# Kernel optimization log

Measured on AMD Instinct MI355X. Metric: run time of the kernel, lower is better.

## Reference

```python
import jax, jax.numpy as jnp
import numpy as np

N = 100000
E = 1600000
D = 128
EPS = 1e-5


def setup_inputs() -> dict:
    key = jax.random.key(0)
    ks = jax.random.split(key, 6)
    X = jax.random.normal(ks[0], (N, D), dtype=jnp.float32)
    edge_weight = jax.random.uniform(ks[1], (E,), dtype=jnp.float32)
    W = jax.random.normal(ks[2], (2 * D, D), dtype=jnp.float32) * (1.0 / np.sqrt(2 * D))
    b = jax.random.normal(ks[3], (D,), dtype=jnp.float32) * 0.01
    gamma = jnp.ones((D,), dtype=jnp.float32)
    beta = jnp.zeros((D,), dtype=jnp.float32)
    edge_src = jax.random.randint(ks[4], (E,), 0, N, dtype=jnp.int32)
    edge_dst = jax.random.randint(ks[5], (E,), 0, N, dtype=jnp.int32)
    return {"X": X, "edge_weight": edge_weight, "W": W, "b": b,
            "gamma": gamma, "beta": beta,
            "edge_src": edge_src, "edge_dst": edge_dst}


def reference(X, edge_weight, W, b, gamma, beta, edge_src, edge_dst):
    # Pre-LayerNorm over feature dim
    mu = jnp.mean(X, axis=-1, keepdims=True)
    var = jnp.mean(jnp.square(X - mu), axis=-1, keepdims=True)
    H = (X - mu) * jax.lax.rsqrt(var + EPS) * gamma + beta
    # dropout is identity in eval mode
    # sparse neighbor aggregation: neigh[i] = sum_{e: dst[e]=i} w[e] * H[src[e]]
    msgs = edge_weight[:, None] * H[edge_src]          # [E, D]
    neigh = jax.ops.segment_sum(msgs, edge_dst, num_segments=X.shape[0])  # [N, D]
    cat = jnp.concatenate([H, neigh], axis=1)          # [N, 2D]
    out = cat @ W + b                                  # [N, D]
    out = jax.nn.relu(out)
    return out + X                                     # residual (in_dim == out_dim)
```

## Files before the change

kernel.cpp:

```cpp
#include <hip/hip_runtime.h>
#include <hip/hip_bf16.h>

#define N_NODES 100000
#define D 128
#define E_EDGES 1600000

#define BSHIFT 6
#define BROWS 64
#define NBUCK 1563
#define CAP 1536
#define NBLK_S 256
#define EPB (E_EDGES / NBLK_S)
#define LN_BLOCKS (N_NODES / 4)

typedef __attribute__((ext_vector_type(8))) short bf16x8;
typedef __attribute__((ext_vector_type(4))) float f32x4;

__device__ __forceinline__ float bf2f(unsigned short u) {
    unsigned int x = ((unsigned int)u) << 16;
    return __builtin_bit_cast(float, x);
}
__device__ __forceinline__ unsigned short f2bf(float f) {
    unsigned int x = __builtin_bit_cast(unsigned int, f);
    unsigned int lsb = (x >> 16) & 1u;
    x += 0x7fffu + lsb;
    return (unsigned short)(x >> 16);
}

__global__ __launch_bounds__(256) void fused_ln_scatter(
    const float* __restrict__ X,
    const float* __restrict__ gamma,
    const float* __restrict__ beta,
    unsigned short* __restrict__ H,
    const int* __restrict__ esrc, const int* __restrict__ edst,
    const float* __restrict__ ew,
    unsigned int* __restrict__ gcur,
    uint2* __restrict__ bins)
{
    __shared__ unsigned int h[NBUCK];

    if (blockIdx.x < NBLK_S) {
        const int t = threadIdx.x;
        for (int i = t; i < NBUCK; i += 256) h[i] = 0;
        __syncthreads();

        const int base = blockIdx.x * EPB;
        for (int k = t; k < EPB; k += 256)
            atomicAdd(&h[edst[base + k] >> BSHIFT], 1u);
        __syncthreads();

        for (int i = t; i < NBUCK; i += 256) {
            unsigned int c = h[i];
            h[i] = c ? atomicAdd(&gcur[i], c) : 0u;
        }
        __syncthreads();

        for (int k = t; k < EPB; k += 256) {
            int e = base + k;
            int d = edst[e];
            int bkt = d >> BSHIFT;
            unsigned int p = atomicAdd(&h[bkt], 1u);
            if (p < CAP)
                bins[(size_t)bkt * CAP + p] =
                    make_uint2((unsigned int)esrc[e] |
                               ((unsigned int)(d & (BROWS - 1)) << 17),
                               __builtin_bit_cast(unsigned int, ew[e]));
        }
    } else {
        int wid  = ((blockIdx.x - NBLK_S) * 256 + threadIdx.x) >> 6;
        int lane = threadIdx.x & 63;
        if (wid >= N_NODES) return;

        const float2 x2 = *reinterpret_cast<const float2*>(X + (size_t)wid * D + 2 * lane);
        float x0 = x2.x, x1 = x2.y;
        float s  = x0 + x1;
        float sq = x0 * x0 + x1 * x1;
        #pragma unroll
        for (int m = 1; m < 64; m <<= 1) {
            s  += __shfl_xor(s,  m);
            sq += __shfl_xor(sq, m);
        }
        float mu   = s * (1.0f / 128.0f);
        float var  = sq * (1.0f / 128.0f) - mu * mu;
        float rstd = rsqrtf(var + 1e-5f);

        const float2 g2 = *reinterpret_cast<const float2*>(gamma + 2 * lane);
        const float2 b2 = *reinterpret_cast<const float2*>(beta  + 2 * lane);

        ushort2 h2;
        h2.x = f2bf((x0 - mu) * rstd * g2.x + b2.x);
        h2.y = f2bf((x1 - mu) * rstd * g2.y + b2.y);
        *reinterpret_cast<ushort2*>(H + (size_t)wid * D + 2 * lane) = h2;
    }
}

__global__ __launch_bounds__(256) void bucket_sort(
    uint2* __restrict__ bins,
    const unsigned int* __restrict__ gcur,
    uint2* __restrict__ offs2)
{
    __shared__ uint2 ent[CAP];
    __shared__ unsigned int cnt[BROWS];
    __shared__ unsigned int cur[BROWS];

    const int b = blockIdx.x;
    const int t = threadIdx.x;
    const unsigned int e0 = (unsigned int)b * CAP;
    const int nE = (int)min(gcur[b], (unsigned int)CAP);

    if (t < BROWS) cnt[t] = 0;
    __syncthreads();

    for (int k = t; k < nE; k += 256) {
        uint2 r = bins[e0 + k];
        ent[k] = r;
        atomicAdd(&cnt[r.x >> 17], 1u);
    }
    __syncthreads();

    if (t < BROWS) {
        unsigned int v = cnt[t], inc = v;
        #pragma unroll
        for (int off = 1; off < BROWS; off <<= 1) {
            unsigned int u = __shfl_up(inc, off);
            if (t >= off) inc += u;
        }
        unsigned int start = e0 + inc - v;
        cur[t] = start;
        int node = b * BROWS + t;
        if (node < N_NODES) offs2[node] = make_uint2(start, start + v);
    }
    __syncthreads();

    for (int k = t; k < nE; k += 256) {
        uint2 r = ent[k];
        unsigned int p = atomicAdd(&cur[r.x >> 17], 1u);
        bins[p] = make_uint2(r.x & 0x1FFFFu, r.y);
    }
}

__global__ __launch_bounds__(256) void aggregate_kernel(
    const unsigned short* __restrict__ H,
    const uint2* __restrict__ bins,
    const uint2* __restrict__ offs2,
    unsigned short* __restrict__ nb)
{
    int wid  = (blockIdx.x * blockDim.x + threadIdx.x) >> 6;
    int lane = threadIdx.x & 63;
    if (wid >= N_NODES) return;

    const uint2 o = offs2[wid];
    unsigned int e = o.x, e1 = o.y;
    float a0 = 0.f, a1 = 0.f;

    while (e + 8 <= e1) {
        uint2 r[8];
        #pragma unroll
        for (int j = 0; j < 8; ++j) r[j] = bins[e + j];
        ushort2 hh[8];
        #pragma unroll
        for (int j = 0; j < 8; ++j)
            hh[j] = *reinterpret_cast<const ushort2*>(H + (size_t)r[j].x * D + 2 * lane);
        #pragma unroll
        for (int j = 0; j < 8; ++j) {
            float w = __builtin_bit_cast(float, r[j].y);
            a0 += w * bf2f(hh[j].x);
            a1 += w * bf2f(hh[j].y);
        }
        e += 8;
    }
    if (e + 4 <= e1) {
        uint2 r[4];
        #pragma unroll
        for (int j = 0; j < 4; ++j) r[j] = bins[e + j];
        #pragma unroll
        for (int j = 0; j < 4; ++j) {
            float w = __builtin_bit_cast(float, r[j].y);
            ushort2 hh = *reinterpret_cast<const ushort2*>(H + (size_t)r[j].x * D + 2 * lane);
            a0 += w * bf2f(hh.x);
            a1 += w * bf2f(hh.y);
        }
        e += 4;
    }
    for (; e < e1; ++e) {
        uint2 r0 = bins[e];
        float w0 = __builtin_bit_cast(float, r0.y);
        ushort2 h0 = *reinterpret_cast<const ushort2*>(H + (size_t)r0.x * D + 2 * lane);
        a0 += w0 * bf2f(h0.x);
        a1 += w0 * bf2f(h0.y);
    }
    ushort2 ov;
    ov.x = f2bf(a0);
    ov.y = f2bf(a1);
    *reinterpret_cast<ushort2*>(nb + (size_t)wid * D + 2 * lane) = ov;
}

#define ROWS_PER_BLOCK 128
#define STRIPS 8

__global__ __launch_bounds__(256) void gemm_kernel(
    const unsigned short* __restrict__ H,
    const unsigned short* __restrict__ nb,
    const float* __restrict__ W,
    const float* __restrict__ bias,
    const float* __restrict__ X,
    float* __restrict__ out)
{
    __shared__ unsigned short lds[16][256];

    const int tid  = threadIdx.x;
    const int w    = tid >> 6;
    const int lane = tid & 63;
    const int l15  = lane & 15;
    const int l4   = lane >> 4;

    bf16x8 bfrag[2][8];
    #pragma unroll
    for (int t = 0; t < 2; ++t) {
        int col = 32 * w + 16 * t + l15;
        #pragma unroll
        for (int s = 0; s < 8; ++s) {
            bf16x8 v;
            #pragma unroll
            for (int j = 0; j < 8; ++j)
                v[j] = (short)f2bf(W[(32 * s + 8 * l4 + j) * D + col]);
            bfrag[t][s] = v;
        }
    }
    const float bias0 = bias[32 * w + l15];
    const float bias1 = bias[32 * w + 16 + l15];

    const int row0_blk = blockIdx.x * ROWS_PER_BLOCK;

    for (int strip = 0; strip < STRIPS; ++strip) {
        const int r0 = row0_blk + strip * 16;
        __syncthreads();

        {
            const int row  = tid >> 4;
            const int c8   = tid & 15;
            const int grow = r0 + row;
            char* ldsrow = (char*)&lds[row][0];
            const int key = (row & 7) << 4;

            uint4 hv = make_uint4(0u, 0u, 0u, 0u);
            uint4 nv = make_uint4(0u, 0u, 0u, 0u);
            if (grow < N_NODES) {
                hv = *reinterpret_cast<const uint4*>(H  + (size_t)grow * D + 8 * c8);
                nv = *reinterpret_cast<const uint4*>(nb + (size_t)grow * D + 8 * c8);
            }
            *reinterpret_cast<uint4*>(ldsrow + ((16 * c8) ^ key)) = hv;
            *reinterpret_cast<uint4*>(ldsrow + ((256 + 16 * c8) ^ key)) = nv;
        }
        __syncthreads();

        f32x4 acc0 = {0.f, 0.f, 0.f, 0.f};
        f32x4 acc1 = {0.f, 0.f, 0.f, 0.f};
        const char* ldsa = (const char*)&lds[l15][0];
        const int   akey = (l15 & 7) << 4;
        #pragma unroll
        for (int s = 0; s < 8; ++s) {
            bf16x8 afrag = *reinterpret_cast<const bf16x8*>(
                ldsa + ((64 * s + 16 * l4) ^ akey));
            acc0 = __builtin_amdgcn_mfma_f32_16x16x32_bf16(afrag, bfrag[0][s], acc0, 0, 0, 0);
            acc1 = __builtin_amdgcn_mfma_f32_16x16x32_bf16(afrag, bfrag[1][s], acc1, 0, 0, 0);
        }

        #pragma unroll
        for (int r = 0; r < 4; ++r) {
            const int grow = r0 + 4 * l4 + r;
            if (grow < N_NODES) {
                const size_t base = (size_t)grow * D;
                const int c0 = 32 * w + l15;
                float v0 = acc0[r] + bias0;
                v0 = v0 > 0.f ? v0 : 0.f;
                out[base + c0] = v0 + X[base + c0];
                const int c1 = c0 + 16;
                float v1 = acc1[r] + bias1;
                v1 = v1 > 0.f ? v1 : 0.f;
                out[base + c1] = v1 + X[base + c1];
            }
        }
    }
}

extern "C" void kernel_launch(void* const* d_in, const int* in_sizes, int n_in,
                              void* d_out, int out_size, void* d_ws, size_t ws_size,
                              hipStream_t stream)
{
    const float* X     = (const float*)d_in[0];
    const float* ew    = (const float*)d_in[1];
    const float* W     = (const float*)d_in[2];
    const float* b     = (const float*)d_in[3];
    const float* gamma = (const float*)d_in[4];
    const float* beta  = (const float*)d_in[5];
    const int* esrc = (const int*)d_in[6];
    const int* edst = (const int*)d_in[7];
    float* out = (float*)d_out;

    unsigned short* H  = (unsigned short*)d_ws;
    unsigned short* nb = H + (size_t)N_NODES * D;
    uint2* bins = (uint2*)(nb + (size_t)N_NODES * D);
    unsigned int* gcur = (unsigned int*)(bins + (size_t)NBUCK * CAP);
    uint2* offs2 = (uint2*)(gcur + NBUCK + 1);

    hipMemsetAsync(gcur, 0, NBUCK * sizeof(unsigned int), stream);
    fused_ln_scatter<<<NBLK_S + LN_BLOCKS, 256, 0, stream>>>(
        X, gamma, beta, H, esrc, edst, ew, gcur, bins);
    bucket_sort<<<NBUCK, 256, 0, stream>>>(bins, gcur, offs2);
    aggregate_kernel<<<N_NODES / 4, 256, 0, stream>>>(H, bins, offs2, nb);
    gemm_kernel<<<(N_NODES + ROWS_PER_BLOCK - 1) / ROWS_PER_BLOCK, 256, 0, stream>>>(
        H, nb, W, b, X, out);
}
```

Measured before the change: 162.6 us.

## Split aggregation wave into two edge halves with 8-byte gathers; pre-convert W to bf16

The aggregation kernel now splits each 64-lane wave into two halves. Each half processes alternate edges and gathers 4 bf16 features (8 bytes) per lane instead of 2, and the halves are combined with a cross-lane shuffle before a single half writes the result. Separately, an extra block in the first kernel converts and transposes W to bf16 once, so each GEMM block loads B fragments with vector loads instead of many strided fp32 loads plus conversions. The goal is fewer, wider gather transactions and a cheaper GEMM prologue. The cost is an added shuffle reduction, half the lanes idle at the store, and the odd tail edge is loaded redundantly by the second half.

New measurement: 178.6 us. 9.8% more time.

```diff
diff --git a/kernel.cpp b/kernel.cpp
--- a/kernel.cpp
+++ b/kernel.cpp
@@ -35,7 +35,9 @@
     const int* __restrict__ esrc, const int* __restrict__ edst,
     const float* __restrict__ ew,
     unsigned int* __restrict__ gcur,
-    uint2* __restrict__ bins)
+    uint2* __restrict__ bins,
+    const float* __restrict__ W,
+    unsigned short* __restrict__ Wt)
 {
     __shared__ unsigned int h[NBUCK];
 
@@ -66,7 +68,7 @@
                                ((unsigned int)(d & (BROWS - 1)) << 17),
                                __builtin_bit_cast(unsigned int, ew[e]));
         }
-    } else {
+    } else if (blockIdx.x < NBLK_S + LN_BLOCKS) {
         int wid  = ((blockIdx.x - NBLK_S) * 256 + threadIdx.x) >> 6;
         int lane = threadIdx.x & 63;
         if (wid >= N_NODES) return;
@@ -91,6 +93,11 @@
         h2.x = f2bf((x0 - mu) * rstd * g2.x + b2.x);
         h2.y = f2bf((x1 - mu) * rstd * g2.y + b2.y);
         *reinterpret_cast<ushort2*>(H + (size_t)wid * D + 2 * lane) = h2;
+    } else {
+        for (int i = threadIdx.x; i < 2 * D * D; i += 256) {
+            int k = i >> 7, col = i & 127;
+            Wt[col * 256 + k] = f2bf(W[i]);
+        }
     }
 }
 
@@ -148,51 +155,58 @@
     int wid  = (blockIdx.x * blockDim.x + threadIdx.x) >> 6;
     int lane = threadIdx.x & 63;
     if (wid >= N_NODES) return;
+    const int half = lane >> 5;
+    const int l31  = lane & 31;
 
     const uint2 o = offs2[wid];
-    unsigned int e = o.x, e1 = o.y;
-    float a0 = 0.f, a1 = 0.f;
-
-    while (e + 8 <= e1) {
-        uint2 r[8];
-        #pragma unroll
-        for (int j = 0; j < 8; ++j) r[j] = bins[e + j];
-        ushort2 hh[8];
-        #pragma unroll
-        for (int j = 0; j < 8; ++j)
-            hh[j] = *reinterpret_cast<const ushort2*>(H + (size_t)r[j].x * D + 2 * lane);
-        #pragma unroll
-        for (int j = 0; j < 8; ++j) {
-            float w = __builtin_bit_cast(float, r[j].y);
-            a0 += w * bf2f(hh[j].x);
-            a1 += w * bf2f(hh[j].y);
-        }
-        e += 8;
-    }
-    if (e + 4 <= e1) {
+    const unsigned int e = o.x;
+    const int n = (int)(o.y - o.x);
+
+    float a0 = 0.f, a1 = 0.f, a2 = 0.f, a3 = 0.f;
+
+    int k = 0;
+    for (; k + 8 <= n; k += 8) {
         uint2 r[4];
         #pragma unroll
-        for (int j = 0; j < 4; ++j) r[j] = bins[e + j];
+        for (int j = 0; j < 4; ++j) r[j] = bins[e + k + 2 * j + half];
+        ushort4 h[4];
+        #pragma unroll
+        for (int j = 0; j < 4; ++j)
+            h[j] = *reinterpret_cast<const ushort4*>(H + (size_t)r[j].x * D + 4 * l31);
         #pragma unroll
         for (int j = 0; j < 4; ++j) {
             float w = __builtin_bit_cast(float, r[j].y);
-            ushort2 hh = *reinterpret_cast<const ushort2*>(H + (size_t)r[j].x * D + 2 * lane);
-            a0 += w * bf2f(hh.x);
-            a1 += w * bf2f(hh.y);
-        }
-        e += 4;
-    }
-    for (; e < e1; ++e) {
-        uint2 r0 = bins[e];
-        float w0 = __builtin_bit_cast(float, r0.y);
-        ushort2 h0 = *reinterpret_cast<const ushort2*>(H + (size_t)r0.x * D + 2 * lane);
-        a0 += w0 * bf2f(h0.x);
-        a1 += w0 * bf2f(h0.y);
-    }
-    ushort2 ov;
-    ov.x = f2bf(a0);
-    ov.y = f2bf(a1);
-    *reinterpret_cast<ushort2*>(nb + (size_t)wid * D + 2 * lane) = ov;
+            a0 += w * bf2f(h[j].x);
+            a1 += w * bf2f(h[j].y);
+            a2 += w * bf2f(h[j].z);
+            a3 += w * bf2f(h[j].w);
+        }
+    }
+    for (; k + 2 <= n; k += 2) {
+        uint2 r = bins[e + k + half];
+        float w = __builtin_bit_cast(float, r.y);
+        ushort4 h = *reinterpret_cast<const ushort4*>(H + (size_t)r.x * D + 4 * l31);
+        a0 += w * bf2f(h.x); a1 += w * bf2f(h.y);
+        a2 += w * bf2f(h.z); a3 += w * bf2f(h.w);
+    }
+    if (k < n) {
+        uint2 r = bins[e + k];
+        float w = half ? 0.f : __builtin_bit_cast(float, r.y);
+        ushort4 h = *reinterpret_cast<const ushort4*>(H + (size_t)r.x * D + 4 * l31);
+        a0 += w * bf2f(h.x); a1 += w * bf2f(h.y);
+        a2 += w * bf2f(h.z); a3 += w * bf2f(h.w);
+    }
+
+    a0 += __shfl_xor(a0, 32);
+    a1 += __shfl_xor(a1, 32);
+    a2 += __shfl_xor(a2, 32);
+    a3 += __shfl_xor(a3, 32);
+
+    if (half == 0) {
+        ushort4 ov;
+        ov.x = f2bf(a0); ov.y = f2bf(a1); ov.z = f2bf(a2); ov.w = f2bf(a3);
+        *reinterpret_cast<ushort4*>(nb + (size_t)wid * D + 4 * l31) = ov;
+    }
 }
 
 #define ROWS_PER_BLOCK 128
@@ -201,7 +215,7 @@
 __global__ __launch_bounds__(256) void gemm_kernel(
     const unsigned short* __restrict__ H,
     const unsigned short* __restrict__ nb,
-    const float* __restrict__ W,
+    const unsigned short* __restrict__ Wt,
     const float* __restrict__ bias,
     const float* __restrict__ X,
     float* __restrict__ out)
@@ -217,15 +231,11 @@
     bf16x8 bfrag[2][8];
     #pragma unroll
     for (int t = 0; t < 2; ++t) {
-        int col = 32 * w + 16 * t + l15;
-        #pragma unroll
-        for (int s = 0; s < 8; ++s) {
-            bf16x8 v;
-            #pragma unroll
-            for (int j = 0; j < 8; ++j)
-                v[j] = (short)f2bf(W[(32 * s + 8 * l4 + j) * D + col]);
-            bfrag[t][s] = v;
-        }
+        const int col = 32 * w + 16 * t + l15;
+        #pragma unroll
+        for (int s = 0; s < 8; ++s)
+            bfrag[t][s] = *reinterpret_cast<const bf16x8*>(
+                Wt + (size_t)col * 256 + 32 * s + 8 * l4);
     }
     const float bias0 = bias[32 * w + l15];
     const float bias1 = bias[32 * w + 16 + l15];
@@ -303,12 +313,13 @@
     uint2* bins = (uint2*)(nb + (size_t)N_NODES * D);
     unsigned int* gcur = (unsigned int*)(bins + (size_t)NBUCK * CAP);
     uint2* offs2 = (uint2*)(gcur + NBUCK + 1);
+    unsigned short* Wt = (unsigned short*)(offs2 + N_NODES);
 
     hipMemsetAsync(gcur, 0, NBUCK * sizeof(unsigned int), stream);
-    fused_ln_scatter<<<NBLK_S + LN_BLOCKS, 256, 0, stream>>>(
-        X, gamma, beta, H, esrc, edst, ew, gcur, bins);
+    fused_ln_scatter<<<NBLK_S + LN_BLOCKS + 1, 256, 0, stream>>>(
+        X, gamma, beta, H, esrc, edst, ew, gcur, bins, W, Wt);
     bucket_sort<<<NBUCK, 256, 0, stream>>>(bins, gcur, offs2);
-    aggregate_kernel<<<N_NODES / 4, 256, 0, stream>>>(H, bins, offs2, nb);
+    aggregate_kernel<<<(N_NODES + 3) / 4, 256, 0, stream>>>(H, bins, offs2, nb);
     gemm_kernel<<<(N_NODES + ROWS_PER_BLOCK - 1) / ROWS_PER_BLOCK, 256, 0, stream>>>(
-        H, nb, W, b, X, out);
-}
+        H, nb, Wt, b, X, out);
+}
```
